# Performance work log

Hardware: AMD Instinct MI355X
Metric: run time of the kernel (lower is better)

The kernel has to match this reference:

```python
import jax, jax.numpy as jnp
import numpy as np

HIDDEN = 768
HEADS = 12
NCH = 3

def setup_inputs() -> dict:
    key = jax.random.key(0)
    ks = jax.random.split(key, 8)
    B, S, D = 16, 512, HIDDEN
    Ht = jax.random.normal(ks[0], (B, S, D), dtype=jnp.float32)
    M_list = jax.random.uniform(ks[1], (B, NCH, S, S), dtype=jnp.float32)
    attention_mask = jnp.ones((B, S), dtype=jnp.float32)
    sc = 1.0 / np.sqrt(D)
    W_qk = jax.random.normal(ks[2], (D, 2 * D), dtype=jnp.float32) * sc
    b_qk = jnp.zeros((2 * D,), dtype=jnp.float32)
    W_gat = jax.random.normal(ks[3], (NCH, D, D), dtype=jnp.float32) * sc
    b_gat = jnp.zeros((NCH, D), dtype=jnp.float32)
    return {"Ht": Ht, "M_list": M_list, "attention_mask": attention_mask,
            "W_qk": W_qk, "b_qk": b_qk, "W_gat": W_gat, "b_gat": b_gat}

def reference(Ht, M_list, attention_mask, W_qk, b_qk, W_gat, b_gat):
    B, S, D = Ht.shape
    dh = D // HEADS
    # text self-attention
    qk = Ht @ W_qk + b_qk                                   # (B,S,2D)
    Q, K = jnp.split(qk, 2, axis=-1)
    Q = Q.reshape(B, S, HEADS, dh).transpose(0, 2, 1, 3)    # (B,H,S,dh)
    K = K.reshape(B, S, HEADS, dh).transpose(0, 2, 1, 3)
    scores = jnp.einsum('bhqd,bhkd->bhqk', Q, K) / jnp.sqrt(jnp.float32(D))
    scores = scores + (1.0 - attention_mask)[:, None, None, :] * (-1e9)
    P = jax.nn.softmax(scores, axis=-1)                     # (B,H,S,S)
    # pairwise mask
    mask_matrix = attention_mask[:, :, None] * attention_mask[:, None, :]  # (B,S,S)
    Mp = jnp.transpose(M_list, (1, 0, 2, 3))                # (h,B,S,S)
    feats = []
    for i in range(NCH):
        M = Mp[i] * mask_matrix                             # (B,S,S)
        A = M[:, None, :, :] * P                            # (B,H,S,S)
        A = A / (A.sum(axis=-1, keepdims=True) + 1e-10)
        feat = jnp.einsum('bqk,bkd->bqd', A.mean(axis=1), Ht)
        feat = jax.nn.relu(feat @ W_gat[i] + b_gat[i])      # (B,S,D)
        feats.append(feat * attention_mask[:, :, None])
    H_fusion = jnp.stack(feats).mean(axis=0)
    return H_fusion
```

## Files before the change

### kernel.cpp

```cpp
#include <hip/hip_runtime.h>
#include <math.h>

typedef __attribute__((ext_vector_type(8))) short short8;
typedef __attribute__((ext_vector_type(4))) float floatx4;

#define TB 16
#define TS 512
#define TD 768
#define TH 12
#define TDH 64
#define TNCH 3

#define SCALE 0.03608439182435161f

__device__ __forceinline__ unsigned short f2bf(float f) {
  unsigned u = __float_as_uint(f);
  u += 0x7fffu + ((u >> 16) & 1u);
  return (unsigned short)(u >> 16);
}
__device__ __forceinline__ unsigned f2bf2(float lo, float hi) {
  return (unsigned)f2bf(lo) | ((unsigned)f2bf(hi) << 16);
}

union U4 { uint4 u; short8 s; };

__global__ __launch_bounds__(256)
void pfuse(const float* __restrict__ src, unsigned short* __restrict__ drm,
           unsigned short* __restrict__ dtr, int R, int C) {
  __shared__ float ts[32][33];
  const size_t zoff = (size_t)blockIdx.z * R * C;
  src += zoff; drm += zoff; dtr += zoff;
  const int c0 = blockIdx.x * 32, r0 = blockIdx.y * 32;
  const int x = threadIdx.x & 31, y = threadIdx.x >> 5;
#pragma unroll
  for (int i = 0; i < 4; i++) {
    const float v = src[(size_t)(r0 + y + 8 * i) * C + c0 + x];
    ts[y + 8 * i][x] = v;
    drm[(size_t)(r0 + y + 8 * i) * C + c0 + x] = f2bf(v);
  }
  __syncthreads();
#pragma unroll
  for (int i = 0; i < 4; i++)
    dtr[(size_t)(c0 + y + 8 * i) * R + r0 + x] = f2bf(ts[x][y + 8 * i]);
}

__global__ __launch_bounds__(256)
void ptrans(const float* __restrict__ src, unsigned short* __restrict__ dst,
            int R, int C) {
  __shared__ float ts[32][33];
  const size_t zoff = (size_t)blockIdx.z * R * C;
  src += zoff; dst += zoff;
  const int c0 = blockIdx.x * 32, r0 = blockIdx.y * 32;
  const int x = threadIdx.x & 31, y = threadIdx.x >> 5;
#pragma unroll
  for (int i = 0; i < 4; i++)
    ts[y + 8 * i][x] = src[(size_t)(r0 + y + 8 * i) * C + c0 + x];
  __syncthreads();
#pragma unroll
  for (int i = 0; i < 4; i++)
    dst[(size_t)(c0 + y + 8 * i) * R + r0 + x] = f2bf(ts[x][y + 8 * i]);
}

__device__ __forceinline__ void stage_gll(const unsigned short* __restrict__ S, int ld,
                                          int row0, int k0, int w, int lane,
                                          unsigned short* D) {
  const int rsub = lane >> 2, c = lane & 3;
#pragma unroll
  for (int i = 0; i < 2; i++) {
    const int r = w * 32 + i * 16;
    const unsigned short* g = &S[(size_t)(row0 + r + rsub) * ld + k0 + c * 8];
    unsigned short* d = &D[r * 32];
    __builtin_amdgcn_global_load_lds(
        (const __attribute__((address_space(1))) unsigned int*)(const void*)g,
        (__attribute__((address_space(3))) unsigned int*)(void*)d,
        16, 0, 0);
  }
}

__device__ __forceinline__ void mfma_step_lin(const unsigned short* As, const unsigned short* Bs,
                                              int wy, int wx, int l16, int quad,
                                              floatx4 acc[4][4]) {
  short8 af[4], bfr[4];
#pragma unroll
  for (int i = 0; i < 4; i++) {
    U4 t; t.u = *(const uint4*)&As[(wy * 64 + i * 16 + l16) * 32 + quad * 8];
    af[i] = t.s;
  }
#pragma unroll
  for (int j = 0; j < 4; j++) {
    U4 t; t.u = *(const uint4*)&Bs[(wx * 64 + j * 16 + l16) * 32 + quad * 8];
    bfr[j] = t.s;
  }
#pragma unroll
  for (int i = 0; i < 4; i++)
#pragma unroll
    for (int j = 0; j < 4; j++)
      acc[i][j] = __builtin_amdgcn_mfma_f32_16x16x32_bf16(af[i], bfr[j], acc[i][j], 0, 0, 0);
}

__device__ __forceinline__ int xcd_chunk(int bid, int cpx) {
  return (bid & 7) * cpx + (bid >> 3);
}

__global__ __launch_bounds__(256, 2)
void k1_qk(const unsigned short* __restrict__ Htb, const unsigned short* __restrict__ WqkT,
           const float* __restrict__ bias, unsigned short* __restrict__ Q,
           unsigned short* __restrict__ Ko) {
  __shared__ unsigned short As0[128 * 32], As1[128 * 32];
  __shared__ unsigned short Bs0[128 * 32], Bs1[128 * 32];
  const int tid = threadIdx.x;
  const int t = xcd_chunk(blockIdx.x, 96);
  const int row0 = (t / 12) * 128, col0 = (t % 12) * 128;
  const int w = tid >> 6, lane = tid & 63;
  const int wy = w >> 1, wx = w & 1, l16 = lane & 15, quad = lane >> 4;
  floatx4 acc[4][4];
#pragma unroll
  for (int i = 0; i < 4; i++)
#pragma unroll
    for (int j = 0; j < 4; j++)
#pragma unroll
      for (int r = 0; r < 4; r++) acc[i][j][r] = 0.f;

  for (int k0 = 0; k0 < TD; k0 += 64) {
    stage_gll(Htb, TD, row0, k0, w, lane, As0);
    stage_gll(WqkT, TD, col0, k0, w, lane, Bs0);
    stage_gll(Htb, TD, row0, k0 + 32, w, lane, As1);
    stage_gll(WqkT, TD, col0, k0 + 32, w, lane, Bs1);
    __syncthreads();
    mfma_step_lin(As0, Bs0, wy, wx, l16, quad, acc);
    mfma_step_lin(As1, Bs1, wy, wx, l16, quad, acc);
    __syncthreads();
  }
#pragma unroll
  for (int i = 0; i < 4; i++)
#pragma unroll
    for (int j = 0; j < 4; j++) {
      const int col = col0 + wx * 64 + j * 16 + l16;
      const float bs = bias[col];
#pragma unroll
      for (int r = 0; r < 4; r++) {
        const int row = row0 + wy * 64 + i * 16 + quad * 4 + r;
        const float v = acc[i][j][r] + bs;
        if (col < TD) Q[(size_t)row * TD + col] = f2bf(v);
        else          Ko[(size_t)row * TD + (col - TD)] = f2bf(v);
      }
    }
}

#define OB_S 520
__global__ __launch_bounds__(256, 2)
void k2_attn(const unsigned short* __restrict__ Q, const unsigned short* __restrict__ Kb,
             const float* __restrict__ Ml, const float* __restrict__ am,
             unsigned short* __restrict__ Am) {
  __shared__ float4 ldsf4[1040];
  const int i0 = blockIdx.x;
  const int xcd = i0 & 7, jj = i0 >> 3;
  const int b = xcd + 8 * (jj & 1);
  const int q0 = (jj >> 1) * 16;
  const int tid = threadIdx.x;
  const int w = tid >> 6, lane = tid & 63;
  const int l16 = lane & 15, quad = lane >> 4;
  const int kbase = w * 128;

  const float* amb = am + b * TS;
  float amq[4], amk[8], maskv[8];
#pragma unroll
  for (int r = 0; r < 4; r++) amq[r] = amb[q0 + quad * 4 + r];
#pragma unroll
  for (int kt = 0; kt < 8; kt++) {
    amk[kt] = amb[kbase + kt * 16 + l16];
    maskv[kt] = (1.f - amk[kt]) * (-1e9f);
  }

  unsigned Mpk[TNCH][4][4];
#pragma unroll
  for (int i = 0; i < TNCH; i++)
#pragma unroll
    for (int r = 0; r < 4; r++) {
      const float* Mrow = Ml + ((size_t)((b * TNCH + i) * TS + q0 + quad * 4 + r)) * TS;
#pragma unroll
      for (int kt2 = 0; kt2 < 4; kt2++) {
        const int ke = kbase + kt2 * 32 + l16;
        const float me = Mrow[ke] * amk[kt2 * 2] * amq[r];
        const float mo = Mrow[ke + 16] * amk[kt2 * 2 + 1] * amq[r];
        Mpk[i][r][kt2] = f2bf2(me, mo);
      }
    }

  const unsigned short* qbase = Q + ((size_t)(b * TS + q0 + l16)) * TD + quad * 8;
  const unsigned short* kb0   = Kb + ((size_t)(b * TS + kbase + l16)) * TD + quad * 8;

  for (int h = 0; h < TH; h++) {
    floatx4 sacc[8];
#pragma unroll
    for (int kt = 0; kt < 8; kt++)
#pragma unroll
      for (int r = 0; r < 4; r++) sacc[kt][r] = 0.f;
#pragma unroll
    for (int dk = 0; dk < 2; dk++) {
      U4 a; a.u = *(const uint4*)(qbase + h * TDH + dk * 32);
#pragma unroll
      for (int kt = 0; kt < 8; kt++) {
        U4 bb; bb.u = *(const uint4*)(kb0 + (size_t)kt * 16 * TD + h * TDH + dk * 32);
        sacc[kt] = __builtin_amdgcn_mfma_f32_16x16x32_bf16(a.s, bb.s, sacc[kt], 0, 0, 0);
      }
    }
    float e[8][4];
    float Zp[4] = {0.f, 0.f, 0.f, 0.f};
#pragma unroll
    for (int kt = 0; kt < 8; kt++)
#pragma unroll
      for (int r = 0; r < 4; r++) {
        const float v = __expf(sacc[kt][r] * SCALE + maskv[kt]);
        e[kt][r] = v;
        Zp[r] += v;
      }
    float dmp[TNCH][4];
#pragma unroll
    for (int i = 0; i < TNCH; i++)
#pragma unroll
      for (int r = 0; r < 4; r++) {
        float d = 0.f;
#pragma unroll
        for (int kt2 = 0; kt2 < 4; kt2++) {
          const unsigned u = Mpk[i][r][kt2];
          d += __uint_as_float(u << 16) * e[kt2 * 2][r];
          d += __uint_as_float(u & 0xffff0000u) * e[kt2 * 2 + 1][r];
        }
        dmp[i][r] = d;
      }
#pragma unroll
    for (int r = 0; r < 4; r++) {
#pragma unroll
      for (int off = 1; off < 16; off <<= 1) {
        Zp[r] += __shfl_xor(Zp[r], off);
        dmp[0][r] += __shfl_xor(dmp[0][r], off);
        dmp[1][r] += __shfl_xor(dmp[1][r], off);
        dmp[2][r] += __shfl_xor(dmp[2][r], off);
      }
    }
    if (l16 == 0) {
#pragma unroll
      for (int r = 0; r < 4; r++)
        ldsf4[(h * 16 + quad * 4 + r) * 4 + w] =
            make_float4(Zp[r], dmp[0][r], dmp[1][r], dmp[2][r]);
    }
  }
  __syncthreads();

  if (tid < TH * 16) {
    const int h = tid >> 4, q = tid & 15;
    const int base = (h * 16 + q) * 4;
    const float4 p0 = ldsf4[base + 0];
    const float4 p1 = ldsf4[base + 1];
    const float4 p2 = ldsf4[base + 2];
    const float4 p3 = ldsf4[base + 3];
    const float Z  = p0.x + p1.x + p2.x + p3.x;
    const float d0 = p0.y + p1.y + p2.y + p3.y;
    const float d1 = p0.z + p1.z + p2.z + p3.z;
    const float d2 = p0.w + p1.w + p2.w + p3.w;
    const float ez = 1e-10f * Z + 1e-30f;
    ldsf4[768 + h * 16 + q] =
        make_float4(1.f / (d0 + ez), 1.f / (d1 + ez), 1.f / (d2 + ez), 0.f);
  }
  __syncthreads();

  float acc[TNCH][8][4];
#pragma unroll
  for (int i = 0; i < TNCH; i++)
#pragma unroll
    for (int kt = 0; kt < 8; kt++)
#pragma unroll
      for (int r = 0; r < 4; r++) acc[i][kt][r] = 0.f;

  for (int h = 0; h < TH; h++) {
    floatx4 sacc[8];
#pragma unroll
    for (int kt = 0; kt < 8; kt++)
#pragma unroll
      for (int r = 0; r < 4; r++) sacc[kt][r] = 0.f;
#pragma unroll
    for (int dk = 0; dk < 2; dk++) {
      U4 a; a.u = *(const uint4*)(qbase + h * TDH + dk * 32);
#pragma unroll
      for (int kt = 0; kt < 8; kt++) {
        U4 bb; bb.u = *(const uint4*)(kb0 + (size_t)kt * 16 * TD + h * TDH + dk * 32);
        sacc[kt] = __builtin_amdgcn_mfma_f32_16x16x32_bf16(a.s, bb.s, sacc[kt], 0, 0, 0);
      }
    }
    float4 wv[4];
#pragma unroll
    for (int r = 0; r < 4; r++) wv[r] = ldsf4[768 + h * 16 + quad * 4 + r];
#pragma unroll
    for (int kt = 0; kt < 8; kt++)
#pragma unroll
      for (int r = 0; r < 4; r++) {
        const float v = __expf(sacc[kt][r] * SCALE + maskv[kt]);
        acc[0][kt][r] += v * wv[r].x;
        acc[1][kt][r] += v * wv[r].y;
        acc[2][kt][r] += v * wv[r].z;
      }
  }
  __syncthreads();

  unsigned short* obuf = (unsigned short*)ldsf4;
  const float inv_h = 1.f / (float)TH;
  for (int i = 0; i < TNCH; i++) {
#pragma unroll
    for (int r = 0; r < 4; r++) {
      const int q = q0 + quad * 4 + r;
      const float* Mrow = Ml + ((size_t)((b * TNCH + i) * TS + q)) * TS;
#pragma unroll
      for (int kt = 0; kt < 8; kt++) {
        const int k = kbase + kt * 16 + l16;
        const float mv = Mrow[k] * amk[kt] * amq[r];
        obuf[(quad * 4 + r) * OB_S + k] = f2bf(mv * acc[i][kt][r] * inv_h);
      }
    }
    __syncthreads();
#pragma unroll
    for (int it = 0; it < 4; it++) {
      const int idx = tid + it * 256;
      const int row = idx >> 6, c16 = idx & 63;
      const uint4 v = *(const uint4*)&obuf[row * OB_S + c16 * 8];
      *(uint4*)&Am[((size_t)((i * TB + b) * TS + q0 + row)) * TS + c16 * 8] = v;
    }
    __syncthreads();
  }
}

__global__ __launch_bounds__(256, 2)
void k3_feat(const unsigned short* __restrict__ Am, const unsigned short* __restrict__ HtbT,
             unsigned short* __restrict__ G) {
  __shared__ unsigned short As0[128 * 32], As1[128 * 32];
  __shared__ unsigned short Bs0[128 * 32], Bs1[128 * 32];
  const int t = xcd_chunk(blockIdx.x, 144);
  const int z = t / 24;
  const int rc = t % 24;
  const int row0 = (rc / 6) * 128, col0 = (rc % 6) * 128;
  const int b = z & 15;
  const unsigned short* A  = Am + (size_t)z * TS * TS;
  const unsigned short* Bt = HtbT + (size_t)b * TD * TS;
  unsigned short* C = G + (size_t)z * TS * TD;
  const int tid = threadIdx.x;
  const int w = tid >> 6, lane = tid & 63;
  const int wy = w >> 1, wx = w & 1, l16 = lane & 15, quad = lane >> 4;
  floatx4 acc[4][4];
#pragma unroll
  for (int i = 0; i < 4; i++)
#pragma unroll
    for (int j = 0; j < 4; j++)
#pragma unroll
      for (int r = 0; r < 4; r++) acc[i][j][r] = 0.f;

  for (int k0 = 0; k0 < TS; k0 += 64) {
    stage_gll(A, TS, row0, k0, w, lane, As0);
    stage_gll(Bt, TS, col0, k0, w, lane, Bs0);
    stage_gll(A, TS, row0, k0 + 32, w, lane, As1);
    stage_gll(Bt, TS, col0, k0 + 32, w, lane, Bs1);
    __syncthreads();
    mfma_step_lin(As0, Bs0, wy, wx, l16, quad, acc);
    mfma_step_lin(As1, Bs1, wy, wx, l16, quad, acc);
    __syncthreads();
  }
#pragma unroll
  for (int i = 0; i < 4; i++)
#pragma unroll
    for (int j = 0; j < 4; j++) {
      const int col = col0 + wx * 64 + j * 16 + l16;
#pragma unroll
      for (int r = 0; r < 4; r++) {
        const int row = row0 + wy * 64 + i * 16 + quad * 4 + r;
        C[(size_t)row * TD + col] = f2bf(acc[i][j][r]);
      }
    }
}

__global__ __launch_bounds__(256, 2)
void k4_out(const unsigned short* __restrict__ G, const unsigned short* __restrict__ WgT,
            const float* __restrict__ bg, const float* __restrict__ am,
            float* __restrict__ out) {
  __shared__ unsigned short As0[128 * 32], As1[128 * 32];
  __shared__ unsigned short Bs0[128 * 32], Bs1[128 * 32];
  const int tid = threadIdx.x;
  const int t = xcd_chunk(blockIdx.x, 48);
  const int row0 = (t / 6) * 128, col0 = (t % 6) * 128;
  const int w = tid >> 6, lane = tid & 63;
  const int wy = w >> 1, wx = w & 1, l16 = lane & 15, quad = lane >> 4;
  float osum[4][4][4];
#pragma unroll
  for (int i = 0; i < 4; i++)
#pragma unroll
    for (int j = 0; j < 4; j++)
#pragma unroll
      for (int r = 0; r < 4; r++) osum[i][j][r] = 0.f;

  for (int ch = 0; ch < TNCH; ch++) {
    const unsigned short* A  = G + (size_t)ch * (TB * TS) * TD;
    const unsigned short* Bt = WgT + (size_t)ch * TD * TD;
    floatx4 acc[4][4];
#pragma unroll
    for (int i = 0; i < 4; i++)
#pragma unroll
      for (int j = 0; j < 4; j++)
#pragma unroll
        for (int r = 0; r < 4; r++) acc[i][j][r] = 0.f;

    for (int k0 = 0; k0 < TD; k0 += 64) {
      stage_gll(A, TD, row0, k0, w, lane, As0);
      stage_gll(Bt, TD, col0, k0, w, lane, Bs0);
      stage_gll(A, TD, row0, k0 + 32, w, lane, As1);
      stage_gll(Bt, TD, col0, k0 + 32, w, lane, Bs1);
      __syncthreads();
      mfma_step_lin(As0, Bs0, wy, wx, l16, quad, acc);
      mfma_step_lin(As1, Bs1, wy, wx, l16, quad, acc);
      __syncthreads();
    }
#pragma unroll
    for (int i = 0; i < 4; i++)
#pragma unroll
      for (int j = 0; j < 4; j++) {
        const int col = col0 + wx * 64 + j * 16 + l16;
        const float bs = bg[ch * TD + col];
#pragma unroll
        for (int r = 0; r < 4; r++)
          osum[i][j][r] += fmaxf(acc[i][j][r] + bs, 0.f);
      }
  }
#pragma unroll
  for (int i = 0; i < 4; i++)
#pragma unroll
    for (int r = 0; r < 4; r++) {
      const int row = row0 + wy * 64 + i * 16 + quad * 4 + r;
      const float amr = am[row] * (1.f / 3.f);
#pragma unroll
      for (int j = 0; j < 4; j++) {
        const int col = col0 + wx * 64 + j * 16 + l16;
        out[(size_t)row * TD + col] = osum[i][j][r] * amr;
      }
    }
}

extern "C" void kernel_launch(void* const* d_in, const int* in_sizes, int n_in,
                              void* d_out, int out_size, void* d_ws, size_t ws_size,
                              hipStream_t stream) {
  const float* Ht    = (const float*)d_in[0];
  const float* Ml    = (const float*)d_in[1];
  const float* am    = (const float*)d_in[2];
  const float* W_qk  = (const float*)d_in[3];
  const float* b_qk  = (const float*)d_in[4];
  const float* W_gat = (const float*)d_in[5];
  const float* b_gat = (const float*)d_in[6];
  float* out = (float*)d_out;

  unsigned short* base = (unsigned short*)d_ws;
  const size_t SEG = (size_t)TB * TS * TD;
  unsigned short* Q    = base;
  unsigned short* Kw   = base + SEG;
  unsigned short* Htb  = base + 2 * SEG;
  unsigned short* HtbT = base + 3 * SEG;
  unsigned short* WqkT = base + 4 * SEG;
  unsigned short* WgT  = WqkT + (size_t)TD * 2 * TD;
  unsigned short* Am   = WgT + (size_t)TNCH * TD * TD;
  unsigned short* G    = base;

  pfuse <<<dim3(24, 16, 16), 256, 0, stream>>>(Ht, Htb, HtbT, TS, TD);
  ptrans<<<dim3(48, 24, 1),  256, 0, stream>>>(W_qk, WqkT, TD, 2 * TD);
  ptrans<<<dim3(24, 24, 3),  256, 0, stream>>>(W_gat, WgT, TD, TD);

  k1_qk  <<<dim3(768),  256, 0, stream>>>(Htb, WqkT, b_qk, Q, Kw);
  k2_attn<<<dim3(512),  256, 0, stream>>>(Q, Kw, Ml, am, Am);
  k3_feat<<<dim3(1152), 256, 0, stream>>>(Am, HtbT, G);
  k4_out <<<dim3(384),  256, 0, stream>>>(G, WgT, b_gat, am, out);
}
```

Before: 344.3 us.

## Reassociate channel matmuls: precompute Ht·W_gat per channel, then apply attention

Uses associativity to compute (A·Ht)·W as A·(Ht·W). k3 now multiplies Ht by each channel's W_gat and writes the result transposed through LDS, and k4 multiplies the attention matrix by that product, with bias, ReLU and the channel mean applied in k4. The FLOP count stays about the same, but the separate transposed copy of Ht is no longer needed, so the Ht prep collapses to a plain vectorized bf16 convert. The intermediates are reused as workspace in Q/K buffers. The bf16 rounding point changes, since Ht·W is rounded before the attention product.

```diff
diff --git a/kernel.cpp b/kernel.cpp
--- a/kernel.cpp
+++ b/kernel.cpp
@@ -25,23 +25,14 @@
 union U4 { uint4 u; short8 s; };
 
 __global__ __launch_bounds__(256)
-void pfuse(const float* __restrict__ src, unsigned short* __restrict__ drm,
-           unsigned short* __restrict__ dtr, int R, int C) {
-  __shared__ float ts[32][33];
-  const size_t zoff = (size_t)blockIdx.z * R * C;
-  src += zoff; drm += zoff; dtr += zoff;
-  const int c0 = blockIdx.x * 32, r0 = blockIdx.y * 32;
-  const int x = threadIdx.x & 31, y = threadIdx.x >> 5;
-#pragma unroll
-  for (int i = 0; i < 4; i++) {
-    const float v = src[(size_t)(r0 + y + 8 * i) * C + c0 + x];
-    ts[y + 8 * i][x] = v;
-    drm[(size_t)(r0 + y + 8 * i) * C + c0 + x] = f2bf(v);
-  }
-  __syncthreads();
-#pragma unroll
-  for (int i = 0; i < 4; i++)
-    dtr[(size_t)(c0 + y + 8 * i) * R + r0 + x] = f2bf(ts[x][y + 8 * i]);
+void pconv(const float* __restrict__ src, unsigned short* __restrict__ dst) {
+  const int i = (blockIdx.x * 256 + threadIdx.x) * 8;
+  const float4 a = *(const float4*)&src[i];
+  const float4 b = *(const float4*)&src[i + 4];
+  uint4 o;
+  o.x = f2bf2(a.x, a.y); o.y = f2bf2(a.z, a.w);
+  o.z = f2bf2(b.x, b.y); o.w = f2bf2(b.z, b.w);
+  *(uint4*)&dst[i] = o;
 }
 
 __global__ __launch_bounds__(256)
@@ -330,19 +321,21 @@
 }
 
 __global__ __launch_bounds__(256, 2)
-void k3_feat(const unsigned short* __restrict__ Am, const unsigned short* __restrict__ HtbT,
-             unsigned short* __restrict__ G) {
-  __shared__ unsigned short As0[128 * 32], As1[128 * 32];
-  __shared__ unsigned short Bs0[128 * 32], Bs1[128 * 32];
+void k3_htw(const unsigned short* __restrict__ Htb, const unsigned short* __restrict__ WgT,
+            unsigned short* __restrict__ h0, unsigned short* __restrict__ h1,
+            unsigned short* __restrict__ h2) {
+  __shared__ unsigned short shmem[17536];
+  unsigned short* As0 = shmem;
+  unsigned short* Bs0 = shmem + 4096;
+  unsigned short* As1 = shmem + 8192;
+  unsigned short* Bs1 = shmem + 12288;
+  const int tid = threadIdx.x;
   const int t = xcd_chunk(blockIdx.x, 144);
-  const int z = t / 24;
-  const int rc = t % 24;
+  const int ch = t / 384;
+  const int rc = t % 384;
   const int row0 = (rc / 6) * 128, col0 = (rc % 6) * 128;
-  const int b = z & 15;
-  const unsigned short* A  = Am + (size_t)z * TS * TS;
-  const unsigned short* Bt = HtbT + (size_t)b * TD * TS;
-  unsigned short* C = G + (size_t)z * TS * TD;
-  const int tid = threadIdx.x;
+  const unsigned short* Bt = WgT + (size_t)ch * TD * TD;
+  unsigned short* H = (ch == 0) ? h0 : (ch == 1) ? h1 : h2;
   const int w = tid >> 6, lane = tid & 63;
   const int wy = w >> 1, wx = w & 1, l16 = lane & 15, quad = lane >> 4;
   floatx4 acc[4][4];
@@ -353,38 +346,55 @@
 #pragma unroll
       for (int r = 0; r < 4; r++) acc[i][j][r] = 0.f;
 
-  for (int k0 = 0; k0 < TS; k0 += 64) {
-    stage_gll(A, TS, row0, k0, w, lane, As0);
-    stage_gll(Bt, TS, col0, k0, w, lane, Bs0);
-    stage_gll(A, TS, row0, k0 + 32, w, lane, As1);
-    stage_gll(Bt, TS, col0, k0 + 32, w, lane, Bs1);
+  for (int k0 = 0; k0 < TD; k0 += 64) {
+    stage_gll(Htb, TD, row0, k0, w, lane, As0);
+    stage_gll(Bt, TD, col0, k0, w, lane, Bs0);
+    stage_gll(Htb, TD, row0, k0 + 32, w, lane, As1);
+    stage_gll(Bt, TD, col0, k0 + 32, w, lane, Bs1);
     __syncthreads();
     mfma_step_lin(As0, Bs0, wy, wx, l16, quad, acc);
     mfma_step_lin(As1, Bs1, wy, wx, l16, quad, acc);
     __syncthreads();
   }
-#pragma unroll
-  for (int i = 0; i < 4; i++)
-#pragma unroll
-    for (int j = 0; j < 4; j++) {
-      const int col = col0 + wx * 64 + j * 16 + l16;
-#pragma unroll
-      for (int r = 0; r < 4; r++) {
-        const int row = row0 + wy * 64 + i * 16 + quad * 4 + r;
-        C[(size_t)row * TD + col] = f2bf(acc[i][j][r]);
-      }
-    }
+  unsigned short* lds_t = shmem;
+#pragma unroll
+  for (int i = 0; i < 4; i++)
+#pragma unroll
+    for (int j = 0; j < 4; j++)
+#pragma unroll
+      for (int r = 0; r < 4; r++)
+        lds_t[(wy * 64 + i * 16 + quad * 4 + r) * 137 + wx * 64 + j * 16 + l16] =
+            f2bf(acc[i][j][r]);
+  __syncthreads();
+  const int b = row0 >> 9, s0 = row0 & 511;
+#pragma unroll
+  for (int it = 0; it < 8; it++) {
+    const int idx = tid + it * 256;
+    const int d_i = idx >> 4, chunk = idx & 15;
+    unsigned v[4];
+#pragma unroll
+    for (int e = 0; e < 4; e++) {
+      const unsigned short lo = lds_t[(chunk * 8 + 2 * e) * 137 + d_i];
+      const unsigned short hi = lds_t[(chunk * 8 + 2 * e + 1) * 137 + d_i];
+      v[e] = (unsigned)lo | ((unsigned)hi << 16);
+    }
+    *(uint4*)&H[((size_t)(b * TD + col0 + d_i)) * TS + s0 + chunk * 8] =
+        make_uint4(v[0], v[1], v[2], v[3]);
+  }
 }
 
 __global__ __launch_bounds__(256, 2)
-void k4_out(const unsigned short* __restrict__ G, const unsigned short* __restrict__ WgT,
-            const float* __restrict__ bg, const float* __restrict__ am,
-            float* __restrict__ out) {
+void k4_outn(const unsigned short* __restrict__ Am,
+             const unsigned short* __restrict__ h0, const unsigned short* __restrict__ h1,
+             const unsigned short* __restrict__ h2,
+             const float* __restrict__ bg, const float* __restrict__ am,
+             float* __restrict__ out) {
   __shared__ unsigned short As0[128 * 32], As1[128 * 32];
   __shared__ unsigned short Bs0[128 * 32], Bs1[128 * 32];
   const int tid = threadIdx.x;
   const int t = xcd_chunk(blockIdx.x, 48);
   const int row0 = (t / 6) * 128, col0 = (t % 6) * 128;
+  const int b = row0 >> 9, q0_ = row0 & 511;
   const int w = tid >> 6, lane = tid & 63;
   const int wy = w >> 1, wx = w & 1, l16 = lane & 15, quad = lane >> 4;
   float osum[4][4][4];
@@ -396,8 +406,8 @@
       for (int r = 0; r < 4; r++) osum[i][j][r] = 0.f;
 
   for (int ch = 0; ch < TNCH; ch++) {
-    const unsigned short* A  = G + (size_t)ch * (TB * TS) * TD;
-    const unsigned short* Bt = WgT + (size_t)ch * TD * TD;
+    const unsigned short* A  = Am + (size_t)(ch * TB + b) * TS * TS;
+    const unsigned short* Bt = ((ch == 0) ? h0 : (ch == 1) ? h1 : h2) + (size_t)b * TD * TS;
     floatx4 acc[4][4];
 #pragma unroll
     for (int i = 0; i < 4; i++)
@@ -406,11 +416,11 @@
 #pragma unroll
         for (int r = 0; r < 4; r++) acc[i][j][r] = 0.f;
 
-    for (int k0 = 0; k0 < TD; k0 += 64) {
-      stage_gll(A, TD, row0, k0, w, lane, As0);
-      stage_gll(Bt, TD, col0, k0, w, lane, Bs0);
-      stage_gll(A, TD, row0, k0 + 32, w, lane, As1);
-      stage_gll(Bt, TD, col0, k0 + 32, w, lane, Bs1);
+    for (int k0 = 0; k0 < TS; k0 += 64) {
+      stage_gll(A, TS, q0_, k0, w, lane, As0);
+      stage_gll(Bt, TS, col0, k0, w, lane, Bs0);
+      stage_gll(A, TS, q0_, k0 + 32, w, lane, As1);
+      stage_gll(Bt, TS, col0, k0 + 32, w, lane, Bs1);
       __syncthreads();
       mfma_step_lin(As0, Bs0, wy, wx, l16, quad, acc);
       mfma_step_lin(As1, Bs1, wy, wx, l16, quad, acc);
@@ -458,18 +468,19 @@
   unsigned short* Q    = base;
   unsigned short* Kw   = base + SEG;
   unsigned short* Htb  = base + 2 * SEG;
-  unsigned short* HtbT = base + 3 * SEG;
+  unsigned short* HtW2 = base + 3 * SEG;
   unsigned short* WqkT = base + 4 * SEG;
   unsigned short* WgT  = WqkT + (size_t)TD * 2 * TD;
   unsigned short* Am   = WgT + (size_t)TNCH * TD * TD;
-  unsigned short* G    = base;
-
-  pfuse <<<dim3(24, 16, 16), 256, 0, stream>>>(Ht, Htb, HtbT, TS, TD);
-  ptrans<<<dim3(48, 24, 1),  256, 0, stream>>>(W_qk, WqkT, TD, 2 * TD);
-  ptrans<<<dim3(24, 24, 3),  256, 0, stream>>>(W_gat, WgT, TD, TD);
+  unsigned short* HtW0 = Q;
+  unsigned short* HtW1 = Kw;
+
+  pconv <<<dim3(3072), 256, 0, stream>>>(Ht, Htb);
+  ptrans<<<dim3(48, 24, 1), 256, 0, stream>>>(W_qk, WqkT, TD, 2 * TD);
+  ptrans<<<dim3(24, 24, 3), 256, 0, stream>>>(W_gat, WgT, TD, TD);
 
   k1_qk  <<<dim3(768),  256, 0, stream>>>(Htb, WqkT, b_qk, Q, Kw);
   k2_attn<<<dim3(512),  256, 0, stream>>>(Q, Kw, Ml, am, Am);
-  k3_feat<<<dim3(1152), 256, 0, stream>>>(Am, HtbT, G);
-  k4_out <<<dim3(384),  256, 0, stream>>>(G, WgT, b_gat, am, out);
-}
+  k3_htw <<<dim3(1152), 256, 0, stream>>>(Htb, WgT, HtW0, HtW1, HtW2);
+  k4_outn<<<dim3(384),  256, 0, stream>>>(Am, HtW0, HtW1, HtW2, b_gat, am, out);
+}
```

Measured after the change: 331.3 us. 3.8% less time.
